# Kernel tuning notes

Hardware: AMD Instinct MI355X
Metric: run time of the kernel (lower is better)

The kernel has to match this reference:

```python
import jax, jax.numpy as jnp
import numpy as np
from jax import lax

B, C, H, W = 8, 64, 128, 128
KS = 3          # kernel size
K = KS * KS     # kernel field = 9
PAD = 1


def conv2d(x, w, b):
    # x: [B,Cin,H,W], w: [Cout,Cin,kh,kw], 'same' 3x3 conv
    y = lax.conv_general_dilated(x, w, window_strides=(1, 1),
                                 padding=((PAD, PAD), (PAD, PAD)),
                                 dimension_numbers=('NCHW', 'OIHW', 'NCHW'))
    return y + b[None, :, None, None]


def modulated_deform_conv(x, offset, mask, weight, bias):
    # x:[B,C,H,W], offset:[B,2K,H,W] (dy,dx per tap), mask:[B,K,H,W]
    Bs, Cin, Hin, Win = x.shape
    off = offset.reshape(Bs, K, 2, Hin, Win)
    ky, kx = jnp.meshgrid(jnp.arange(KS), jnp.arange(KS), indexing='ij')
    ky = ky.reshape(K).astype(x.dtype)   # kernel tap row offsets 0..2
    kx = kx.reshape(K).astype(x.dtype)
    # sampling positions p = p0 + p_k + offset (stride=1, pad=1)
    py = (jnp.arange(Hin, dtype=x.dtype)[None, None, :, None] - PAD
          + ky[None, :, None, None] + off[:, :, 0])            # [B,K,H,W]
    px = (jnp.arange(Win, dtype=x.dtype)[None, None, None, :] - PAD
          + kx[None, :, None, None] + off[:, :, 1])            # [B,K,H,W]

    y0 = jnp.floor(py); x0 = jnp.floor(px)
    ly = py - y0; lx = px - x0                                  # frac parts
    y0i = y0.astype(jnp.int32); x0i = x0.astype(jnp.int32)

    x_flat = x.reshape(Bs, Cin, Hin * Win)

    def gather(iy, ix):
        valid = ((iy >= 0) & (iy < Hin) & (ix >= 0) & (ix < Win))
        flat = (jnp.clip(iy, 0, Hin - 1) * Win + jnp.clip(ix, 0, Win - 1))
        g = jax.vmap(lambda xb, ib: xb[:, ib])(x_flat, flat.reshape(Bs, -1))
        g = g.reshape(Bs, Cin, K, Hin, Win)
        return g * valid[:, None].astype(x.dtype)

    w00 = ((1 - ly) * (1 - lx))[:, None]  # [B,1,K,H,W]
    w01 = ((1 - ly) * lx)[:, None]
    w10 = (ly * (1 - lx))[:, None]
    w11 = (ly * lx)[:, None]

    val = (w00 * gather(y0i, x0i) + w01 * gather(y0i, x0i + 1)
           + w10 * gather(y0i + 1, x0i) + w11 * gather(y0i + 1, x0i + 1))
    val = val * mask[:, None]                                   # modulation
    out = jnp.einsum('ock,bckhw->bohw', weight.reshape(weight.shape[0], Cin, K), val)
    return out + bias[None, :, None, None]


def setup_inputs() -> dict:
    key = jax.random.key(0)
    ks = jax.random.split(key, 7)
    s = 0.05
    return {
        'x': jax.random.normal(ks[0], (B, C, H, W), jnp.float32),
        'w_om': jax.random.normal(ks[1], (3 * K, C, KS, KS), jnp.float32) * s,
        'b_om': jax.random.normal(ks[2], (3 * K,), jnp.float32) * s,
        'w_dc': jax.random.normal(ks[3], (C, C, KS, KS), jnp.float32) * s,
        'b_dc': jax.random.normal(ks[4], (C,), jnp.float32) * s,
        'w_c': jax.random.normal(ks[5], (C, C, KS, KS), jnp.float32) * s,
        'b_c': jax.random.normal(ks[6], (C,), jnp.float32) * s,
    }


def reference(x, w_om, b_om, w_dc, b_dc, w_c, b_c):
    om = conv2d(x, w_om, b_om)                       # [B,3K,H,W]
    offset, mask_raw = om[:, :2 * K], om[:, 2 * K:]
    mask = 2.0 * jax.nn.sigmoid(mask_raw)
    out = modulated_deform_conv(x, offset, mask, w_dc, b_dc)
    act = jnp.where(out > 0, out, 0.2 * out)         # LeakyReLU(0.2)
    return conv2d(act, w_c, b_c) + x
```

## Files before the change

kernel.cpp:

```cpp
#include <hip/hip_runtime.h>
#include <math.h>

#define Bn 8
#define Cn 64
#define Hn 128
#define Wn 128
#define HWn (Hn * Wn)

#define WOM_OFF 0
#define WDC_OFF 18432
#define WC_OFF 55296

typedef __attribute__((ext_vector_type(8))) short short8;
typedef __attribute__((ext_vector_type(4))) float floatx4;

__device__ __forceinline__ float bf2f(short s) {
  return __uint_as_float(((unsigned)(unsigned short)s) << 16);
}
__device__ __forceinline__ short f2bf(float f) {
  unsigned u = __float_as_uint(f);
  u += 0x7fff + ((u >> 16) & 1);
  return (short)(u >> 16);
}

__global__ __launch_bounds__(256) void k_prep_w(
    const float* __restrict__ w_om, const float* __restrict__ w_dc,
    const float* __restrict__ w_c, short* __restrict__ wt) {
  int idx = blockIdx.x * 256 + threadIdx.x;
  if (idx >= 92160) return;
  float v;
  if (idx < WDC_OFF) {
    int e = idx;
    int elem = e & 7, lane = (e >> 3) & 63, mt = (e >> 9) & 1, t = e >> 10;
    int kk = t % 9, cc = t / 9;
    int row = mt * 16 + (lane & 15);
    int cin = cc * 32 + (lane >> 4) * 8 + elem;
    v = (row < 27) ? w_om[(row * 64 + cin) * 9 + kk] : 0.f;
  } else {
    int e = (idx < WC_OFF) ? idx - WDC_OFF : idx - WC_OFF;
    const float* src = (idx < WC_OFF) ? w_dc : w_c;
    int elem = e & 7, lane = (e >> 3) & 63, mt = (e >> 9) & 3, t = e >> 11;
    int kk = t % 9, cc = t / 9;
    int row = mt * 16 + (lane & 15);
    int cin = cc * 32 + (lane >> 4) * 8 + elem;
    v = src[(row * 64 + cin) * 9 + kk];
  }
  wt[idx] = f2bf(v);
}

__global__ __launch_bounds__(256) void k_prep_x(const float* __restrict__ x,
                                                short* __restrict__ xT) {
  __shared__ float tile[64][129];
  const int bid = blockIdx.x;
  const int b = bid & 7, h = bid >> 3;
  const int tid = threadIdx.x;
  const float* xb = x + (size_t)b * 64 * HWn + h * Wn;
  for (int i = tid; i < 8192; i += 256) {
    int c = i >> 7, w = i & 127;
    tile[c][w] = xb[c * HWn + w];
  }
  __syncthreads();
  short* dst = xT + ((size_t)(b * Hn + h) * Wn) * 64;
  for (int i = tid; i < 2048; i += 256) {
    int w = i >> 4, c4 = (i & 15) * 4;
    short4 o;
    o.x = f2bf(tile[c4 + 0][w]);
    o.y = f2bf(tile[c4 + 1][w]);
    o.z = f2bf(tile[c4 + 2][w]);
    o.w = f2bf(tile[c4 + 3][w]);
    *(short4*)(dst + (size_t)w * 64 + c4) = o;
  }
}

__global__ __launch_bounds__(512, 4) void k_omdef(
    const short* __restrict__ xT, const short* __restrict__ wt,
    const float* __restrict__ b_om, const float* __restrict__ b_dc,
    short* __restrict__ actT) {
  __shared__ __attribute__((aligned(16))) short lw[18432];
  __shared__ float som[2][27 * 132];

  const int bid = blockIdx.x;
  const int b = bid & 7;
  const int h0 = (bid >> 3) * 2;
  const int tid = threadIdx.x;
  const int wave = tid >> 6, lane = tid & 63, quad = lane >> 4, lr = lane & 15;
  const short* xb = xT + (size_t)b * HWn * 64;
  const int pxl = wave * 16 + lr;

  floatx4 zf = {0.f, 0.f, 0.f, 0.f};
  const short8 zz = (short8){0, 0, 0, 0, 0, 0, 0, 0};

  {
    const short8* src = (const short8*)(wt + WOM_OFF);
    short8* dst = (short8*)lw;
    for (int i = tid; i < 2304; i += 512) dst[i] = src[i];
  }
  __syncthreads();

  floatx4 aco[2][2] = {{zf, zf}, {zf, zf}};
#pragma unroll 3
  for (int kk = 0; kk < 9; ++kk) {
    int ky = kk / 3, kx = kk - ky * 3;
    int gx = pxl + kx - 1;
    bool okx = ((unsigned)gx < (unsigned)Wn);
    int gxc = min(max(gx, 0), Wn - 1);
#pragma unroll
    for (int cc = 0; cc < 2; ++cc) {
      short8 a0 = *(const short8*)&lw[((cc * 9 + kk) * 2 + 0) * 512 + lane * 8];
      short8 a1 = *(const short8*)&lw[((cc * 9 + kk) * 2 + 1) * 512 + lane * 8];
#pragma unroll
      for (int r = 0; r < 2; ++r) {
        int gy = h0 + r + ky - 1;
        bool ok = okx && ((unsigned)gy < (unsigned)Hn);
        int gyc = min(max(gy, 0), Hn - 1);
        short8 bf = *(const short8*)(xb + (size_t)(gyc * Wn + gxc) * 64 +
                                     cc * 32 + quad * 8);
        if (!ok) bf = zz;
        aco[r][0] = __builtin_amdgcn_mfma_f32_16x16x32_bf16(a0, bf, aco[r][0], 0, 0, 0);
        aco[r][1] = __builtin_amdgcn_mfma_f32_16x16x32_bf16(a1, bf, aco[r][1], 0, 0, 0);
      }
    }
  }
#pragma unroll
  for (int r = 0; r < 2; ++r) {
#pragma unroll
    for (int mt = 0; mt < 2; ++mt) {
#pragma unroll
      for (int rr = 0; rr < 4; ++rr) {
        int co = mt * 16 + quad * 4 + rr;
        if (co < 27) {
          float v = aco[r][mt][rr] + b_om[co];
          if (co >= 18) v = 2.f / (1.f + expf(-v));
          som[r][co * 132 + pxl] = v;
        }
      }
    }
  }
  asm volatile("s_waitcnt lgkmcnt(0)" ::: "memory");

  floatx4 acc[2][4] = {{zf, zf, zf, zf}, {zf, zf, zf, zf}};
  for (int cc = 0; cc < 2; ++cc) {
    __syncthreads();
    {
      const short8* src = (const short8*)(wt + WDC_OFF + cc * 18432);
      short8* dst = (short8*)lw;
      for (int i = tid; i < 2304; i += 512) dst[i] = src[i];
    }
    __syncthreads();
    const int co = cc * 32 + quad * 8;
#pragma unroll 3
    for (int kk = 0; kk < 9; ++kk) {
      short8 am0 = *(const short8*)&lw[(kk * 4 + 0) * 512 + lane * 8];
      short8 am1 = *(const short8*)&lw[(kk * 4 + 1) * 512 + lane * 8];
      short8 am2 = *(const short8*)&lw[(kk * 4 + 2) * 512 + lane * 8];
      short8 am3 = *(const short8*)&lw[(kk * 4 + 3) * 512 + lane * 8];
#pragma unroll
      for (int r = 0; r < 2; ++r) {
        float offy = som[r][(2 * kk) * 132 + pxl];
        float offx = som[r][(2 * kk + 1) * 132 + pxl];
        float m = som[r][(18 + kk) * 132 + pxl];
        float py = (float)(h0 + r - 1 + (kk / 3)) + offy;
        float px_ = (float)(pxl - 1 + (kk % 3)) + offx;
        float fy = floorf(py), fx = floorf(px_);
        float ly = py - fy, lx = px_ - fx;
        int iy0 = (int)fy, ix0 = (int)fx;
        int iy1 = iy0 + 1, ix1 = ix0 + 1;
        bool vy0 = ((unsigned)iy0 < (unsigned)Hn);
        bool vy1 = ((unsigned)iy1 < (unsigned)Hn);
        bool vx0 = ((unsigned)ix0 < (unsigned)Wn);
        bool vx1 = ((unsigned)ix1 < (unsigned)Wn);
        unsigned cy0 = (unsigned)min(max(iy0, 0), Hn - 1);
        unsigned cy1 = (unsigned)min(max(iy1, 0), Hn - 1);
        unsigned cx0 = (unsigned)min(max(ix0, 0), Wn - 1);
        unsigned cx1 = (unsigned)min(max(ix1, 0), Wn - 1);
        unsigned d0 = cy0 * Wn + cx0, d1 = cy0 * Wn + cx1;
        unsigned d2 = cy1 * Wn + cx0, d3 = cy1 * Wn + cx1;
        float u0 = (vy0 && vx0) ? (1.f - ly) * (1.f - lx) * m : 0.f;
        float u1 = (vy0 && vx1) ? (1.f - ly) * lx * m : 0.f;
        float u2 = (vy1 && vx0) ? ly * (1.f - lx) * m : 0.f;
        float u3 = (vy1 && vx1) ? ly * lx * m : 0.f;

        short8 q0 = *(const short8*)(xb + (size_t)d0 * 64 + co);
        short8 q1 = *(const short8*)(xb + (size_t)d1 * 64 + co);
        short8 q2 = *(const short8*)(xb + (size_t)d2 * 64 + co);
        short8 q3 = *(const short8*)(xb + (size_t)d3 * 64 + co);

        short8 bf;
#pragma unroll
        for (int e = 0; e < 8; ++e) {
          float f = u0 * bf2f(q0[e]) + u1 * bf2f(q1[e]) + u2 * bf2f(q2[e]) +
                    u3 * bf2f(q3[e]);
          bf[e] = f2bf(f);
        }
        acc[r][0] = __builtin_amdgcn_mfma_f32_16x16x32_bf16(am0, bf, acc[r][0], 0, 0, 0);
        acc[r][1] = __builtin_amdgcn_mfma_f32_16x16x32_bf16(am1, bf, acc[r][1], 0, 0, 0);
        acc[r][2] = __builtin_amdgcn_mfma_f32_16x16x32_bf16(am2, bf, acc[r][2], 0, 0, 0);
        acc[r][3] = __builtin_amdgcn_mfma_f32_16x16x32_bf16(am3, bf, acc[r][3], 0, 0, 0);
      }
    }
  }

#pragma unroll
  for (int r = 0; r < 2; ++r) {
    short* ab = actT + ((size_t)(b * Hn + h0 + r) * Wn) * 64;
#pragma unroll
    for (int mt = 0; mt < 4; ++mt) {
      int c0 = mt * 16 + quad * 4;
      short4 o;
      float v;
      v = acc[r][mt][0] + b_dc[c0 + 0]; o.x = f2bf(v > 0.f ? v : 0.2f * v);
      v = acc[r][mt][1] + b_dc[c0 + 1]; o.y = f2bf(v > 0.f ? v : 0.2f * v);
      v = acc[r][mt][2] + b_dc[c0 + 2]; o.z = f2bf(v > 0.f ? v : 0.2f * v);
      v = acc[r][mt][3] + b_dc[c0 + 3]; o.w = f2bf(v > 0.f ? v : 0.2f * v);
      *(short4*)(ab + (size_t)pxl * 64 + c0) = o;
    }
  }
}

__global__ __launch_bounds__(512, 4) void k_conv_out(
    const short* __restrict__ actT, const short* __restrict__ wt,
    const float* __restrict__ b_c, const float* __restrict__ x,
    float* __restrict__ out) {
  __shared__ __attribute__((aligned(16))) short lw[18432];

  const int bid = blockIdx.x;
  const int b = bid & 7;
  const int h0 = (bid >> 3) * 2;
  const int tid = threadIdx.x;
  const int wave = tid >> 6, lane = tid & 63, quad = lane >> 4, lr = lane & 15;
  const short* ab = actT + (size_t)b * HWn * 64;
  const int pxl = wave * 16 + lr;

  floatx4 zf = {0.f, 0.f, 0.f, 0.f};
  const short8 zz = (short8){0, 0, 0, 0, 0, 0, 0, 0};
  floatx4 acc[2][4] = {{zf, zf, zf, zf}, {zf, zf, zf, zf}};

  for (int cc = 0; cc < 2; ++cc) {
    if (cc) __syncthreads();
    {
      const short8* src = (const short8*)(wt + WC_OFF + cc * 18432);
      short8* dst = (short8*)lw;
      for (int i = tid; i < 2304; i += 512) dst[i] = src[i];
    }
    __syncthreads();
    const int co = cc * 32 + quad * 8;
#pragma unroll 3
    for (int kk = 0; kk < 9; ++kk) {
      int ky = kk / 3, kx = kk - ky * 3;
      int gx = pxl + kx - 1;
      bool okx = ((unsigned)gx < (unsigned)Wn);
      int gxc = min(max(gx, 0), Wn - 1);
      short8 am0 = *(const short8*)&lw[(kk * 4 + 0) * 512 + lane * 8];
      short8 am1 = *(const short8*)&lw[(kk * 4 + 1) * 512 + lane * 8];
      short8 am2 = *(const short8*)&lw[(kk * 4 + 2) * 512 + lane * 8];
      short8 am3 = *(const short8*)&lw[(kk * 4 + 3) * 512 + lane * 8];
#pragma unroll
      for (int r = 0; r < 2; ++r) {
        int gy = h0 + r + ky - 1;
        bool ok = okx && ((unsigned)gy < (unsigned)Hn);
        int gyc = min(max(gy, 0), Hn - 1);
        short8 bf = *(const short8*)(ab + (size_t)(gyc * Wn + gxc) * 64 + co);
        if (!ok) bf = zz;
        acc[r][0] = __builtin_amdgcn_mfma_f32_16x16x32_bf16(am0, bf, acc[r][0], 0, 0, 0);
        acc[r][1] = __builtin_amdgcn_mfma_f32_16x16x32_bf16(am1, bf, acc[r][1], 0, 0, 0);
        acc[r][2] = __builtin_amdgcn_mfma_f32_16x16x32_bf16(am2, bf, acc[r][2], 0, 0, 0);
        acc[r][3] = __builtin_amdgcn_mfma_f32_16x16x32_bf16(am3, bf, acc[r][3], 0, 0, 0);
      }
    }
  }
  __syncthreads();

  float* ot = (float*)lw;
#pragma unroll
  for (int r = 0; r < 2; ++r) {
    if (r) __syncthreads();
#pragma unroll
    for (int mt = 0; mt < 4; ++mt) {
#pragma unroll
      for (int rr = 0; rr < 4; ++rr) {
        ot[(mt * 16 + quad * 4 + rr) * 132 + pxl] = acc[r][mt][rr];
      }
    }
    __syncthreads();
    const int row = tid >> 3, seg = tid & 7;
    const float bias = b_c[row];
    const size_t gbase =
        ((size_t)(b * 64 + row) * Hn + h0 + r) * Wn + seg * 16;
    const float* xr = x + gbase;
    float* op = out + gbase;
#pragma unroll
    for (int j = 0; j < 4; ++j) {
      floatx4 t = *(const floatx4*)&ot[row * 132 + seg * 16 + j * 4];
      floatx4 xv = *(const floatx4*)&xr[j * 4];
      t = t + xv;
      t[0] += bias; t[1] += bias; t[2] += bias; t[3] += bias;
      *(floatx4*)&op[j * 4] = t;
    }
  }
}

extern "C" void kernel_launch(void* const* d_in, const int* in_sizes, int n_in,
                              void* d_out, int out_size, void* d_ws,
                              size_t ws_size, hipStream_t stream) {
  const float* x = (const float*)d_in[0];
  const float* w_om = (const float*)d_in[1];
  const float* b_om = (const float*)d_in[2];
  const float* w_dc = (const float*)d_in[3];
  const float* b_dc = (const float*)d_in[4];
  const float* w_c = (const float*)d_in[5];
  const float* b_c = (const float*)d_in[6];
  float* out = (float*)d_out;

  short* xT = (short*)d_ws;
  short* actT = xT + (size_t)Bn * HWn * 64;
  short* wt = actT + (size_t)Bn * HWn * 64;

  k_prep_w<<<dim3(360), 256, 0, stream>>>(w_om, w_dc, w_c, wt);
  k_prep_x<<<dim3(1024), 256, 0, stream>>>(x, xT);
  k_omdef<<<dim3(512), 512, 0, stream>>>(xT, wt, b_om, b_dc, actT);
  k_conv_out<<<dim3(512), 512, 0, stream>>>(actT, wt, b_c, x, out);
}
```

Measured before the change: 217.5 us.

## Software-pipeline deformable gathers with inline-asm loads and explicit vmcnt waits

Restructures the deformable-conv inner loop into a flattened 18-step loop over tap and row. The four bilinear gather loads for the next step are issued with inline global_load_dwordx4 asm before the current step's interpolation and MFMAs run, and partial s_waitcnt vmcnt(4) keeps one stage of loads in flight. Offset and weight parameter computation is moved two steps ahead. The aim is to hide gather memory latency behind compute. The cost is more live registers, and the hand-written waitcnt can break if the compiler emits other vector memory ops in between.

```diff
diff --git a/kernel.cpp b/kernel.cpp
--- a/kernel.cpp
+++ b/kernel.cpp
@@ -72,6 +72,13 @@
   }
 }
 
+#define GL16(d, p) \
+  asm volatile("global_load_dwordx4 %0, %1, off" : "=v"(d) : "v"(p))
+#define WAITV4(a, b, c, d) \
+  asm volatile("s_waitcnt vmcnt(4)" : "+v"(a), "+v"(b), "+v"(c), "+v"(d))
+#define WAITV0(a, b, c, d) \
+  asm volatile("s_waitcnt vmcnt(0)" : "+v"(a), "+v"(b), "+v"(c), "+v"(d))
+
 __global__ __launch_bounds__(512, 4) void k_omdef(
     const short* __restrict__ xT, const short* __restrict__ wt,
     const float* __restrict__ b_om, const float* __restrict__ b_dc,
@@ -148,56 +155,91 @@
     }
     __syncthreads();
     const int co = cc * 32 + quad * 8;
-#pragma unroll 3
-    for (int kk = 0; kk < 9; ++kk) {
-      short8 am0 = *(const short8*)&lw[(kk * 4 + 0) * 512 + lane * 8];
-      short8 am1 = *(const short8*)&lw[(kk * 4 + 1) * 512 + lane * 8];
-      short8 am2 = *(const short8*)&lw[(kk * 4 + 2) * 512 + lane * 8];
-      short8 am3 = *(const short8*)&lw[(kk * 4 + 3) * 512 + lane * 8];
-#pragma unroll
-      for (int r = 0; r < 2; ++r) {
-        float offy = som[r][(2 * kk) * 132 + pxl];
-        float offx = som[r][(2 * kk + 1) * 132 + pxl];
-        float m = som[r][(18 + kk) * 132 + pxl];
-        float py = (float)(h0 + r - 1 + (kk / 3)) + offy;
-        float px_ = (float)(pxl - 1 + (kk % 3)) + offx;
-        float fy = floorf(py), fx = floorf(px_);
-        float ly = py - fy, lx = px_ - fx;
-        int iy0 = (int)fy, ix0 = (int)fx;
-        int iy1 = iy0 + 1, ix1 = ix0 + 1;
-        bool vy0 = ((unsigned)iy0 < (unsigned)Hn);
-        bool vy1 = ((unsigned)iy1 < (unsigned)Hn);
-        bool vx0 = ((unsigned)ix0 < (unsigned)Wn);
-        bool vx1 = ((unsigned)ix1 < (unsigned)Wn);
-        unsigned cy0 = (unsigned)min(max(iy0, 0), Hn - 1);
-        unsigned cy1 = (unsigned)min(max(iy1, 0), Hn - 1);
-        unsigned cx0 = (unsigned)min(max(ix0, 0), Wn - 1);
-        unsigned cx1 = (unsigned)min(max(ix1, 0), Wn - 1);
-        unsigned d0 = cy0 * Wn + cx0, d1 = cy0 * Wn + cx1;
-        unsigned d2 = cy1 * Wn + cx0, d3 = cy1 * Wn + cx1;
-        float u0 = (vy0 && vx0) ? (1.f - ly) * (1.f - lx) * m : 0.f;
-        float u1 = (vy0 && vx1) ? (1.f - ly) * lx * m : 0.f;
-        float u2 = (vy1 && vx0) ? ly * (1.f - lx) * m : 0.f;
-        float u3 = (vy1 && vx1) ? ly * lx * m : 0.f;
-
-        short8 q0 = *(const short8*)(xb + (size_t)d0 * 64 + co);
-        short8 q1 = *(const short8*)(xb + (size_t)d1 * 64 + co);
-        short8 q2 = *(const short8*)(xb + (size_t)d2 * 64 + co);
-        short8 q3 = *(const short8*)(xb + (size_t)d3 * 64 + co);
-
-        short8 bf;
-#pragma unroll
-        for (int e = 0; e < 8; ++e) {
-          float f = u0 * bf2f(q0[e]) + u1 * bf2f(q1[e]) + u2 * bf2f(q2[e]) +
-                    u3 * bf2f(q3[e]);
-          bf[e] = f2bf(f);
-        }
-        acc[r][0] = __builtin_amdgcn_mfma_f32_16x16x32_bf16(am0, bf, acc[r][0], 0, 0, 0);
-        acc[r][1] = __builtin_amdgcn_mfma_f32_16x16x32_bf16(am1, bf, acc[r][1], 0, 0, 0);
-        acc[r][2] = __builtin_amdgcn_mfma_f32_16x16x32_bf16(am2, bf, acc[r][2], 0, 0, 0);
-        acc[r][3] = __builtin_amdgcn_mfma_f32_16x16x32_bf16(am3, bf, acc[r][3], 0, 0, 0);
-      }
-    }
+
+    unsigned pd[2][4];
+    float pu[2][4];
+    short8 q[2][4];
+    float us[2][4];
+
+#define PARAM(TT, S)                                                         \
+  {                                                                          \
+    const int kk_ = (TT) >> 1, r_ = (TT) & 1;                                \
+    float offy = som[r_][(2 * kk_) * 132 + pxl];                             \
+    float offx = som[r_][(2 * kk_ + 1) * 132 + pxl];                         \
+    float m = som[r_][(18 + kk_) * 132 + pxl];                               \
+    float py = (float)(h0 + r_ - 1 + (kk_ / 3)) + offy;                      \
+    float px_ = (float)(pxl - 1 + (kk_ % 3)) + offx;                         \
+    float fy = floorf(py), fx = floorf(px_);                                 \
+    float ly = py - fy, lx = px_ - fx;                                       \
+    int iy0 = (int)fy, ix0 = (int)fx;                                        \
+    int iy1 = iy0 + 1, ix1 = ix0 + 1;                                        \
+    bool vy0 = ((unsigned)iy0 < (unsigned)Hn);                               \
+    bool vy1 = ((unsigned)iy1 < (unsigned)Hn);                               \
+    bool vx0 = ((unsigned)ix0 < (unsigned)Wn);                               \
+    bool vx1 = ((unsigned)ix1 < (unsigned)Wn);                               \
+    unsigned cy0 = (unsigned)min(max(iy0, 0), Hn - 1);                       \
+    unsigned cy1 = (unsigned)min(max(iy1, 0), Hn - 1);                       \
+    unsigned cx0 = (unsigned)min(max(ix0, 0), Wn - 1);                       \
+    unsigned cx1 = (unsigned)min(max(ix1, 0), Wn - 1);                       \
+    pd[S][0] = cy0 * Wn + cx0;                                               \
+    pd[S][1] = cy0 * Wn + cx1;                                               \
+    pd[S][2] = cy1 * Wn + cx0;                                               \
+    pd[S][3] = cy1 * Wn + cx1;                                               \
+    pu[S][0] = (vy0 && vx0) ? (1.f - ly) * (1.f - lx) * m : 0.f;             \
+    pu[S][1] = (vy0 && vx1) ? (1.f - ly) * lx * m : 0.f;                     \
+    pu[S][2] = (vy1 && vx0) ? ly * (1.f - lx) * m : 0.f;                     \
+    pu[S][3] = (vy1 && vx1) ? ly * lx * m : 0.f;                             \
+  }
+
+#define ISSUE(S)                                                             \
+  {                                                                          \
+    const short* p0 = xb + (size_t)pd[S][0] * 64 + co;                       \
+    const short* p1 = xb + (size_t)pd[S][1] * 64 + co;                       \
+    const short* p2 = xb + (size_t)pd[S][2] * 64 + co;                       \
+    const short* p3 = xb + (size_t)pd[S][3] * 64 + co;                       \
+    GL16(q[S][0], p0);                                                       \
+    GL16(q[S][1], p1);                                                       \
+    GL16(q[S][2], p2);                                                       \
+    GL16(q[S][3], p3);                                                       \
+    us[S][0] = pu[S][0]; us[S][1] = pu[S][1];                                \
+    us[S][2] = pu[S][2]; us[S][3] = pu[S][3];                                \
+  }
+
+    PARAM(0, 0);
+    PARAM(1, 1);
+    ISSUE(0);
+    short8 am0, am1, am2, am3;
+#pragma unroll
+    for (int t = 0; t < 18; ++t) {
+      const int s = t & 1;
+      if (t < 17) ISSUE((t + 1) & 1);
+      if (t < 16) PARAM(t + 2, s);
+      if (t < 17) {
+        WAITV4(q[s][0], q[s][1], q[s][2], q[s][3]);
+      } else {
+        WAITV0(q[s][0], q[s][1], q[s][2], q[s][3]);
+      }
+      const int kk = t >> 1, r = t & 1;
+      if (r == 0) {
+        am0 = *(const short8*)&lw[(kk * 4 + 0) * 512 + lane * 8];
+        am1 = *(const short8*)&lw[(kk * 4 + 1) * 512 + lane * 8];
+        am2 = *(const short8*)&lw[(kk * 4 + 2) * 512 + lane * 8];
+        am3 = *(const short8*)&lw[(kk * 4 + 3) * 512 + lane * 8];
+      }
+      short8 bf;
+#pragma unroll
+      for (int e = 0; e < 8; ++e) {
+        float f = us[s][0] * bf2f(q[s][0][e]) + us[s][1] * bf2f(q[s][1][e]) +
+                  us[s][2] * bf2f(q[s][2][e]) + us[s][3] * bf2f(q[s][3][e]);
+        bf[e] = f2bf(f);
+      }
+      acc[r][0] = __builtin_amdgcn_mfma_f32_16x16x32_bf16(am0, bf, acc[r][0], 0, 0, 0);
+      acc[r][1] = __builtin_amdgcn_mfma_f32_16x16x32_bf16(am1, bf, acc[r][1], 0, 0, 0);
+      acc[r][2] = __builtin_amdgcn_mfma_f32_16x16x32_bf16(am2, bf, acc[r][2], 0, 0, 0);
+      acc[r][3] = __builtin_amdgcn_mfma_f32_16x16x32_bf16(am3, bf, acc[r][3], 0, 0, 0);
+    }
+#undef PARAM
+#undef ISSUE
   }
 
 #pragma unroll
```

After: 226.4 us. 1.04x slower.
